# Optimization experiments

Measured on AMD Instinct MI355X. Metric: run time of the kernel, lower is better.

The kernel has to match this reference:

```python
import jax, jax.numpy as jnp
import numpy as np

# model constants (from source: PRE/COMM/OUT sizes; chosen: G, D, E, T, NF)
G, D, E, T = 128, 64, 8, 4096          # group feats, per-elevator feats, n elevators, timesteps
PRE, CI, CH, OUT, NF = 256, 128, 128, 128, 64
ROUNDS, DROPOFF = 3, 0.333
IN = G + D                              # elevator_input_size = 192
OIN = 2 * CH + IN                       # out-LSTM input = 448


def _cell(x, h, c, Wih, Whh, b):
    # torch nn.LSTM cell, gate order i,f,g,o; b = b_ih + b_hh
    g = x @ Wih.T + h @ Whh.T + b
    i, f, gg, o = jnp.split(g, 4, axis=-1)
    c2 = jax.nn.sigmoid(f) * c + jax.nn.sigmoid(i) * jnp.tanh(gg)
    h2 = jax.nn.sigmoid(o) * jnp.tanh(c2)
    return h2, c2


def _forward(features, pre_h0, pre_c0, out_h0, out_c0,
             Wih_p0, Whh_p0, b_p0, Wih_p1, Whh_p1, b_p1, Wfc, bfc,
             Wih_c0, Whh_c0, b_c0, Wih_c1, Whh_c1, b_c1,
             Wih_o, Whh_o, b_o, Wtar, btar, Wdir, bdir):
    def step(carry, feat):
        pre_h, pre_c, out_h, out_c = carry
        group = feat[:G]
        ele = feat[G:].reshape(E, D)
        x = jnp.concatenate([jnp.broadcast_to(group, (E, G)), ele], axis=-1)  # [E, IN]
        # preprocess: 2-layer LSTM single step, batched over elevators
        h0, c0 = _cell(x, pre_h[:, 0], pre_c[:, 0], Wih_p0, Whh_p0, b_p0)
        h1, c1 = _cell(h0, pre_h[:, 1], pre_c[:, 1], Wih_p1, Whh_p1, b_p1)
        pre_out = jax.nn.leaky_relu(h1 @ Wfc.T + bfc, 0.05)                   # [E, CI]
        new_pre_h = jnp.stack([h0, h1], axis=1)
        new_pre_c = jnp.stack([c0, c1], axis=1)
        # alpha-decayed communication rounds: sequential scan over elevators
        ch = jnp.zeros((2, CH), jnp.float32)
        cc = jnp.zeros((2, CH), jnp.float32)
        alpha = 1.0
        for _ in range(ROUNDS):
            def comm_step(cs, xin, alpha=alpha):
                ch_, cc_ = cs
                h0n, c0n = _cell(xin, ch_[0], cc_[0], Wih_c0, Whh_c0, b_c0)
                h0b = (1.0 - alpha) * ch_[0] + alpha * h0n
                c0b = (1.0 - alpha) * cc_[0] + alpha * c0n
                h1n, c1n = _cell(h0b, ch_[1], cc_[1], Wih_c1, Whh_c1, b_c1)
                h1b = (1.0 - alpha) * ch_[1] + alpha * h1n
                c1b = (1.0 - alpha) * cc_[1] + alpha * c1n
                return (jnp.stack([h0b, h1b]), jnp.stack([c0b, c1b])), None
            (ch, cc), _ = jax.lax.scan(comm_step, (ch, cc), pre_out)
            alpha *= DROPOFF
        group_dec = cc.reshape(-1)                                            # [2*CH] = comm_c.flatten()
        out_in = jnp.concatenate([jnp.broadcast_to(group_dec, (E, 2 * CH)), x], axis=-1)  # [E, OIN]
        oh, oc = _cell(out_in, out_h, out_c, Wih_o, Whh_o, b_o)
        tar = jax.nn.softmax(oh @ Wtar.T + btar, axis=-1)                     # [E, NF]
        dr = jax.nn.softmax(oh @ Wdir.T + bdir, axis=-1)                      # [E, 3]
        return (new_pre_h, new_pre_c, oh, oc), (tar, dr)

    _, (tar_seq, dir_seq) = jax.lax.scan(step, (pre_h0, pre_c0, out_h0, out_c0), features)
    return tar_seq, dir_seq


def setup_inputs() -> dict:
    key = jax.random.key(0)
    ks = iter(jax.random.split(key, 32))
    p = lambda *s: jax.random.normal(next(ks), s, jnp.float32) * 0.05
    return {
        "features": jax.random.normal(next(ks), (T, G + E * D), jnp.float32),
        "pre_h0": jnp.zeros((E, 2, PRE), jnp.float32),
        "pre_c0": jnp.zeros((E, 2, PRE), jnp.float32),
        "out_h0": jnp.zeros((E, OUT), jnp.float32),
        "out_c0": jnp.zeros((E, OUT), jnp.float32),
        "Wih_p0": p(4 * PRE, IN), "Whh_p0": p(4 * PRE, PRE), "b_p0": p(4 * PRE),
        "Wih_p1": p(4 * PRE, PRE), "Whh_p1": p(4 * PRE, PRE), "b_p1": p(4 * PRE),
        "Wfc": p(CI, PRE), "bfc": p(CI),
        "Wih_c0": p(4 * CH, CI), "Whh_c0": p(4 * CH, CH), "b_c0": p(4 * CH),
        "Wih_c1": p(4 * CH, CH), "Whh_c1": p(4 * CH, CH), "b_c1": p(4 * CH),
        "Wih_o": p(4 * OUT, OIN), "Whh_o": p(4 * OUT, OUT), "b_o": p(4 * OUT),
        "Wtar": p(NF, OUT), "btar": p(NF),
        "Wdir": p(3, OUT), "bdir": p(3),
    }


def reference(features, pre_h0, pre_c0, out_h0, out_c0,
              Wih_p0, Whh_p0, b_p0, Wih_p1, Whh_p1, b_p1, Wfc, bfc,
              Wih_c0, Whh_c0, b_c0, Wih_c1, Whh_c1, b_c1,
              Wih_o, Whh_o, b_o, Wtar, btar, Wdir, bdir):
    return _forward(features, pre_h0, pre_c0, out_h0, out_c0,
                    Wih_p0, Whh_p0, b_p0, Wih_p1, Whh_p1, b_p1, Wfc, bfc,
                    Wih_c0, Whh_c0, b_c0, Wih_c1, Whh_c1, b_c1,
                    Wih_o, Whh_o, b_o, Wtar, btar, Wdir, bdir)
```

## Files before the change

### kernel.cpp

```cpp
#include <hip/hip_runtime.h>
#include <hip/hip_bf16.h>

#define T_   4096
#define E_   8
#define NCON 56

typedef unsigned long long ull;

__device__ __forceinline__ float sigm(float x)  { return 1.0f / (1.0f + __expf(-x)); }
__device__ __forceinline__ float tanh_(float x) { return 1.0f - 2.0f / (__expf(2.0f * x) + 1.0f); }

__device__ __forceinline__ ull aload64(const ull* p) {
  return __hip_atomic_load(p, __ATOMIC_RELAXED, __HIP_MEMORY_SCOPE_AGENT);
}
__device__ __forceinline__ int aload32(const int* p) {
  return __hip_atomic_load(p, __ATOMIC_RELAXED, __HIP_MEMORY_SCOPE_AGENT);
}
__device__ __forceinline__ float aloadf(const float* p) {
  return __hip_atomic_load(p, __ATOMIC_RELAXED, __HIP_MEMORY_SCOPE_AGENT);
}
__device__ __forceinline__ float tagf(float h, unsigned g) {
  return __uint_as_float((__float_as_uint(h) & ~7u) | g);
}
__device__ __forceinline__ bool tagok4(const ull* v, unsigned g) {
  bool ok = true;
  #pragma unroll
  for (int i = 0; i < 4; ++i) {
    unsigned lo = (unsigned)v[i], hi = (unsigned)(v[i] >> 32);
    ok &= ((lo & 7u) == g) & ((hi & 7u) == g);
  }
  return ok;
}
__device__ __forceinline__ void lbar() {
  asm volatile("s_waitcnt lgkmcnt(0)\n\ts_barrier" ::: "memory");
}

#define FMA_8(ACC, W, VA, VB)                                   \
  ACC[0] = fmaf((W), (VA).x, ACC[0]); ACC[1] = fmaf((W), (VA).y, ACC[1]); \
  ACC[2] = fmaf((W), (VA).z, ACC[2]); ACC[3] = fmaf((W), (VA).w, ACC[3]); \
  ACC[4] = fmaf((W), (VB).x, ACC[4]); ACC[5] = fmaf((W), (VB).y, ACC[5]); \
  ACC[6] = fmaf((W), (VB).z, ACC[6]); ACC[7] = fmaf((W), (VB).w, ACC[7]);

__global__ void initK(const float* __restrict__ Wih_p0, const float* __restrict__ Whh_p0,
                      const float* __restrict__ Wih_p1, const float* __restrict__ Whh_p1,
                      const float* __restrict__ Wih_c0, const float* __restrict__ Whh_c0,
                      const float* __restrict__ Wih_c1, const float* __restrict__ Whh_c1,
                      const float* __restrict__ Wih_o,
                      float* wt_p0, float* wt_p1, float* wt_c0, float* wt_c1,
                      float* wt_o1, float* wt_o2, int* zbase) {
  const int NW = 458752 + 524288 + 131072 + 131072 + 131072 + 98304;
  const int NZ = 65536 + 16384 + 65536 + 16384;
  const int NTOT = NW + NZ;
  const int gsz = gridDim.x * blockDim.x;
  for (int i = blockIdx.x * blockDim.x + threadIdx.x; i < NTOT; i += gsz) {
    int idx = i;
    if (idx < 458752) { int k = idx >> 10, c = idx & 1023;
      int wg = c >> 5, r5 = c & 31, gate = r5 >> 3, jl = r5 & 7;
      int col = gate * 256 + wg * 8 + jl;
      wt_p0[idx] = (k < 192) ? Wih_p0[col * 192 + k] : Whh_p0[col * 256 + (k - 192)]; continue; }
    idx -= 458752;
    if (idx < 524288) { int k = idx >> 10, c = idx & 1023;
      int wg = c >> 5, r5 = c & 31, gate = r5 >> 3, jl = r5 & 7;
      int col = gate * 256 + wg * 8 + jl;
      wt_p1[idx] = (k < 256) ? Wih_p1[col * 256 + k] : Whh_p1[col * 256 + (k - 256)]; continue; }
    idx -= 524288;
    if (idx < 131072) { int k = idx >> 9, r = idx & 511;
      wt_c0[idx] = (k < 128) ? Wih_c0[r * 128 + k] : Whh_c0[r * 128 + (k - 128)]; continue; }
    idx -= 131072;
    if (idx < 131072) { int k = idx >> 9, r = idx & 511;
      wt_c1[idx] = (k < 128) ? Wih_c1[r * 128 + k] : Whh_c1[r * 128 + (k - 128)]; continue; }
    idx -= 131072;
    if (idx < 131072) { int k = idx >> 9, r = idx & 511;
      wt_o1[idx] = Wih_o[r * 448 + k]; continue; }
    idx -= 131072;
    if (idx < 98304) { int k = idx >> 9, r = idx & 511;
      wt_o2[idx] = Wih_o[r * 448 + 256 + k]; continue; }
    idx -= 98304;
    zbase[idx] = 0;
  }
}

__global__ void opre2K(const float* __restrict__ feat, const float* __restrict__ wt_o2,
                       __hip_bfloat16* __restrict__ opre2) {
  __shared__ float xb[192 * 8];
  const int t = blockIdx.x, tid = threadIdx.x;
  const float* ft = feat + (size_t)t * 640;
  for (int idx = tid; idx < 192 * 8; idx += 256) {
    int k = idx >> 3, e = idx & 7;
    xb[idx] = (k < 128) ? ft[k] : ft[128 + e * 64 + (k - 128)];
  }
  __syncthreads();
  const int r = tid;
  float A0[8] = {0,0,0,0,0,0,0,0};
  float A1[8] = {0,0,0,0,0,0,0,0};
  const float4* x4 = (const float4*)xb;
  #pragma unroll 2
  for (int k = 0; k < 192; ++k) {
    float w0 = wt_o2[k * 512 + r];
    float w1 = wt_o2[k * 512 + 256 + r];
    float4 a = x4[k * 2], b = x4[k * 2 + 1];
    FMA_8(A0, w0, a, b);
    FMA_8(A1, w1, a, b);
  }
  #pragma unroll
  for (int e = 0; e < 8; ++e) {
    opre2[((size_t)t * 8 + e) * 512 + r]       = __float2bfloat16(A0[e]);
    opre2[((size_t)t * 8 + e) * 512 + 256 + r] = __float2bfloat16(A1[e]);
  }
}

__device__ __forceinline__ void comm_cell(
    const float* __restrict__ wt, const float* __restrict__ bias,
    const float* xin, float* hL, float* cL, float* glb, float* hout,
    float alpha, int tid) {
  const int r = tid;
  float A0[8] = {0,0,0,0,0,0,0,0};
  float A1[8] = {0,0,0,0,0,0,0,0};
  const float4* x4 = (const float4*)xin;
  #pragma unroll 2
  for (int k = 0; k < 128; ++k) {
    float w0 = wt[k * 512 + r];
    float w1 = wt[k * 512 + 256 + r];
    float4 a = x4[k * 2], b = x4[k * 2 + 1];
    FMA_8(A0, w0, a, b);
    FMA_8(A1, w1, a, b);
  }
  const float4* h4 = (const float4*)hL;
  #pragma unroll 2
  for (int k = 0; k < 128; ++k) {
    float w0 = wt[(128 + k) * 512 + r];
    float w1 = wt[(128 + k) * 512 + 256 + r];
    float4 a = h4[k * 2], b = h4[k * 2 + 1];
    FMA_8(A0, w0, a, b);
    FMA_8(A1, w1, a, b);
  }
  {
    float4* g4 = (float4*)glb;
    g4[r * 2]             = make_float4(A0[0], A0[1], A0[2], A0[3]);
    g4[r * 2 + 1]         = make_float4(A0[4], A0[5], A0[6], A0[7]);
    g4[(256 + r) * 2]     = make_float4(A1[0], A1[1], A1[2], A1[3]);
    g4[(256 + r) * 2 + 1] = make_float4(A1[4], A1[5], A1[6], A1[7]);
  }
  __syncthreads();
  for (int idx = tid; idx < 1024; idx += 256) {
    int jj = idx >> 3, tt = idx & 7;
    float gi = glb[jj * 8 + tt]         + bias[jj];
    float gf = glb[(128 + jj) * 8 + tt] + bias[128 + jj];
    float gg = glb[(256 + jj) * 8 + tt] + bias[256 + jj];
    float go = glb[(384 + jj) * 8 + tt] + bias[384 + jj];
    float cold = cL[idx], hold = hL[idx];
    float c2 = sigm(gf) * cold + sigm(gi) * tanh_(gg);
    float h2 = sigm(go) * tanh_(c2);
    float hb = fmaf(alpha, h2 - hold, hold);
    float cb = fmaf(alpha, c2 - cold, cold);
    hL[idx] = hb; cL[idx] = cb;
    if (hout) hout[idx] = hb;
  }
  __syncthreads();
}

__launch_bounds__(256, 1)
__global__ void megaK(const float* __restrict__ feat,
                      const float* __restrict__ pre_h0, const float* __restrict__ pre_c0,
                      const float* __restrict__ wt_p0, const float* __restrict__ wt_p1,
                      const float* __restrict__ b_p0, const float* __restrict__ b_p1,
                      float* __restrict__ h0ring, float* __restrict__ h1ring,
                      float* __restrict__ h1all, int* __restrict__ flagsBC,
                      const float* __restrict__ Wfc, const float* __restrict__ bfc,
                      const float* __restrict__ wt_c0, const float* __restrict__ wt_c1,
                      const float* __restrict__ b_c0, const float* __restrict__ b_c1,
                      const float* __restrict__ wt_o1, const float* __restrict__ b_o,
                      float* __restrict__ opre1, int* __restrict__ flagC,
                      const __hip_bfloat16* __restrict__ opre2,
                      const float* __restrict__ Whh_o, const float* __restrict__ out_h0,
                      const float* __restrict__ out_c0, float* __restrict__ oh_g) {
  __shared__ float lds[38912];
  const int wg = blockIdx.x, tid = threadIdx.x;

  if (wg < 32) {
    float* wl  = lds;
    float* xb0 = lds + 14336;
    float* xb1 = lds + 15872;
    float* hsf = lds + 17408;
    float* gl  = lds + 19456;
    const int r5 = tid & 31, kq = tid >> 5;
    for (int idx = tid; idx < 14336; idx += 256)
      wl[idx] = wt_p0[(size_t)(idx >> 5) * 1024 + wg * 32 + (idx & 31)];
    float creg = 0.f, bi = 0.f, bff = 0.f, bg = 0.f, bo = 0.f;
    if (tid < 64) {
      const int jl = tid >> 3, e = tid & 7, j = wg * 8 + jl;
      creg = pre_c0[(e * 2 + 0) * 256 + j];
      bi = b_p0[j]; bff = b_p0[256 + j]; bg = b_p0[512 + j]; bo = b_p0[768 + j];
    }
    for (int idx = tid; idx < 2048; idx += 256) {
      int k = idx >> 3, e = idx & 7;
      hsf[idx] = pre_h0[(e * 2 + 0) * 256 + k];
    }
    for (int idx = tid; idx < 1536; idx += 256) {
      int k = idx >> 3, e = idx & 7;
      xb0[idx] = (k < 128) ? feat[k] : feat[128 + e * 64 + (k - 128)];
    }
    __syncthreads();
    const bool own = ((tid >> 3) == wg);
    float Ax[8] = {0,0,0,0,0,0,0,0};
    {
      const float4* x4 = (const float4*)xb0;
      #pragma unroll
      for (int k = kq * 24; k < kq * 24 + 24; ++k) {
        float w = wl[k * 32 + r5];
        float4 a = x4[k * 2], b = x4[k * 2 + 1];
        FMA_8(Ax, w, a, b);
      }
    }
    for (int t = 0; t < T_; ++t) {
      float px[6];
      if (t + 1 < T_) {
        const float* ft1 = feat + (size_t)(t + 1) * 640;
        #pragma unroll
        for (int i = 0; i < 6; ++i) {
          int idx = tid + i * 256; int k = idx >> 3, e = idx & 7;
          px[i] = (k < 128) ? ft1[k] : ft1[128 + e * 64 + (k - 128)];
        }
      }
      float A[8];
      #pragma unroll
      for (int i = 0; i < 8; ++i) A[i] = Ax[i];
      {
        const float4* h4 = (const float4*)hsf;
        #pragma unroll
        for (int k2 = 0; k2 < 32; ++k2) {
          const int k = kq * 32 + k2;
          float w = wl[(192 + k) * 32 + r5];
          float4 a = h4[k * 2], b = h4[k * 2 + 1];
          FMA_8(A, w, a, b);
        }
      }
      {
        float4* g4 = (float4*)gl;
        g4[(kq * 32 + r5) * 2]     = make_float4(A[0], A[1], A[2], A[3]);
        g4[(kq * 32 + r5) * 2 + 1] = make_float4(A[4], A[5], A[6], A[7]);
      }
      if (t + 1 < T_) {
        float* xbN = ((t + 1) & 1) ? xb1 : xb0;
        #pragma unroll
        for (int i = 0; i < 6; ++i) xbN[tid + i * 256] = px[i];
      }
      if (t >= 24 && tid >= 224) {
        const int t2 = (t - 24) | 7;
        const int* fp = flagsBC + ((size_t)(t2 & 63) * 32 + (tid - 224)) * 32;
        while (aload32(fp) < t2 + 1) __builtin_amdgcn_s_sleep(16);
      }
      lbar();
      const unsigned g = ((unsigned)(t >> 5) % 7u) + 1u;
      float* ringS = h0ring + (size_t)(t & 31) * 2048;
      if (tid < 64) {
        float s0 = 0.f, s1 = 0.f, s2 = 0.f, s3 = 0.f;
        #pragma unroll
        for (int q = 0; q < 8; ++q) {
          s0 += gl[q * 256 + tid];       s1 += gl[q * 256 + 64 + tid];
          s2 += gl[q * 256 + 128 + tid]; s3 += gl[q * 256 + 192 + tid];
        }
        float c2 = sigm(s1 + bff) * creg + sigm(s0 + bi) * tanh_(s2 + bg);
        float h2 = sigm(s3 + bo) * tanh_(c2);
        creg = c2;
        __hip_atomic_store(&ringS[wg * 64 + tid], tagf(h2, g),
                           __ATOMIC_RELAXED, __HIP_MEMORY_SCOPE_AGENT);
        hsf[wg * 64 + tid] = h2;
      }
      if (t + 1 >= T_) break;
      ull v[4];
      const ull* rp = (const ull*)ringS + tid * 4;
      if (!own) {
        #pragma unroll
        for (int i = 0; i < 4; ++i) v[i] = aload64(rp + i);
      }
      #pragma unroll
      for (int i = 0; i < 8; ++i) Ax[i] = 0.f;
      {
        const float4* x4 = (const float4*)(((t + 1) & 1) ? xb1 : xb0);
        #pragma unroll
        for (int k = kq * 24; k < kq * 24 + 24; ++k) {
          float w = wl[k * 32 + r5];
          float4 a = x4[k * 2], b = x4[k * 2 + 1];
          FMA_8(Ax, w, a, b);
        }
      }
      if (!own) {
        while (!tagok4(v, g)) {
          __builtin_amdgcn_s_sleep(1);
          #pragma unroll
          for (int i = 0; i < 4; ++i) v[i] = aload64(rp + i);
        }
        ull* d8 = (ull*)hsf;
        #pragma unroll
        for (int i = 0; i < 4; ++i) d8[tid * 4 + i] = v[i];
      }
      lbar();
    }
  } else if (wg < 64) {
    const int wgl = wg - 32;
    float* wl  = lds;
    float* xh0 = lds + 16384;
    float* hsf = lds + 18432;
    float* gl  = lds + 20480;
    const int r5 = tid & 31, kq = tid >> 5;
    for (int idx = tid; idx < 16384; idx += 256)
      wl[idx] = wt_p1[(size_t)(idx >> 5) * 1024 + wgl * 32 + (idx & 31)];
    float creg = 0.f, bi = 0.f, bff = 0.f, bg = 0.f, bo = 0.f;
    if (tid < 64) {
      const int jl = tid >> 3, e = tid & 7, j = wgl * 8 + jl;
      creg = pre_c0[(e * 2 + 1) * 256 + j];
      bi = b_p1[j]; bff = b_p1[256 + j]; bg = b_p1[512 + j]; bo = b_p1[768 + j];
    }
    for (int idx = tid; idx < 2048; idx += 256) {
      int k = idx >> 3, e = idx & 7;
      hsf[idx] = pre_h0[(e * 2 + 1) * 256 + k];
    }
    __syncthreads();
    const bool own = ((tid >> 3) == wgl);
    ull pv[4];
    {
      ull v[4];
      const ull* rp = (const ull*)h0ring + tid * 4;
      #pragma unroll
      for (int i = 0; i < 4; ++i) v[i] = aload64(rp + i);
      while (!tagok4(v, 1u)) {
        __builtin_amdgcn_s_sleep(1);
        #pragma unroll
        for (int i = 0; i < 4; ++i) v[i] = aload64(rp + i);
      }
      ull* d8 = (ull*)xh0;
      #pragma unroll
      for (int i = 0; i < 4; ++i) d8[tid * 4 + i] = v[i];
    }
    lbar();
    float Ax[8] = {0,0,0,0,0,0,0,0};
    {
      const float4* x4 = (const float4*)xh0;
      #pragma unroll
      for (int k = kq * 32; k < kq * 32 + 32; ++k) {
        float w = wl[k * 32 + r5];
        float4 a = x4[k * 2], b = x4[k * 2 + 1];
        FMA_8(Ax, w, a, b);
      }
    }
    {
      const ull* rp = (const ull*)(h0ring + 2048) + tid * 4;
      #pragma unroll
      for (int i = 0; i < 4; ++i) pv[i] = aload64(rp + i);
      while (!tagok4(pv, 1u)) {
        __builtin_amdgcn_s_sleep(1);
        #pragma unroll
        for (int i = 0; i < 4; ++i) pv[i] = aload64(rp + i);
      }
    }
    lbar();
    for (int t = 0; t < T_; ++t) {
      float A[8];
      #pragma unroll
      for (int i = 0; i < 8; ++i) A[i] = Ax[i];
      {
        const float4* h4 = (const float4*)hsf;
        #pragma unroll
        for (int k2 = 0; k2 < 32; ++k2) {
          const int k = kq * 32 + k2;
          float w = wl[(256 + k) * 32 + r5];
          float4 a = h4[k * 2], b = h4[k * 2 + 1];
          FMA_8(A, w, a, b);
        }
      }
      {
        float4* g4 = (float4*)gl;
        g4[(kq * 32 + r5) * 2]     = make_float4(A[0], A[1], A[2], A[3]);
        g4[(kq * 32 + r5) * 2 + 1] = make_float4(A[4], A[5], A[6], A[7]);
      }
      if (t + 1 < T_) {
        ull* d8 = (ull*)xh0;
        #pragma unroll
        for (int i = 0; i < 4; ++i) d8[tid * 4 + i] = pv[i];
      }
      lbar();
      const unsigned g1 = ((unsigned)(t >> 3) % 7u) + 1u;
      float* ringS = h1ring + (size_t)(t & 7) * 2048;
      if (tid < 64) {
        float s0 = 0.f, s1 = 0.f, s2 = 0.f, s3 = 0.f;
        #pragma unroll
        for (int q = 0; q < 8; ++q) {
          s0 += gl[q * 256 + tid];       s1 += gl[q * 256 + 64 + tid];
          s2 += gl[q * 256 + 128 + tid]; s3 += gl[q * 256 + 192 + tid];
        }
        float c2 = sigm(s1 + bff) * creg + sigm(s0 + bi) * tanh_(s2 + bg);
        float h2 = sigm(s3 + bo) * tanh_(c2);
        creg = c2;
        __hip_atomic_store(&ringS[wgl * 64 + tid], tagf(h2, g1),
                           __ATOMIC_RELAXED, __HIP_MEMORY_SCOPE_AGENT);
        hsf[wgl * 64 + tid] = h2;
        __hip_atomic_store(&h1all[(size_t)t * 2048 + wgl * 64 + tid], h2,
                           __ATOMIC_RELAXED, __HIP_MEMORY_SCOPE_AGENT);
        if ((t & 7) == 7) {
          asm volatile("s_waitcnt vmcnt(0)" ::: "memory");
          if (tid == 0)
            __hip_atomic_store(&flagsBC[((size_t)(t & 63) * 32 + wgl) * 32], t + 1,
                               __ATOMIC_RELAXED, __HIP_MEMORY_SCOPE_AGENT);
        }
      }
      if (t + 1 >= T_) break;
      ull w1[4];
      const ull* rp1 = (const ull*)ringS + tid * 4;
      if (!own) {
        #pragma unroll
        for (int i = 0; i < 4; ++i) w1[i] = aload64(rp1 + i);
      }
      #pragma unroll
      for (int i = 0; i < 8; ++i) Ax[i] = 0.f;
      {
        const float4* x4 = (const float4*)xh0;
        #pragma unroll
        for (int k = kq * 32; k < kq * 32 + 32; ++k) {
          float w = wl[k * 32 + r5];
          float4 a = x4[k * 2], b = x4[k * 2 + 1];
          FMA_8(Ax, w, a, b);
        }
      }
      if (!own) {
        while (!tagok4(w1, g1)) {
          __builtin_amdgcn_s_sleep(1);
          #pragma unroll
          for (int i = 0; i < 4; ++i) w1[i] = aload64(rp1 + i);
        }
        ull* d8 = (ull*)hsf;
        #pragma unroll
        for (int i = 0; i < 4; ++i) d8[tid * 4 + i] = w1[i];
      }
      if (t + 2 < T_) {
        const unsigned g0 = ((unsigned)((t + 2) >> 5) % 7u) + 1u;
        const ull* rp0 = (const ull*)(h0ring + (size_t)((t + 2) & 31) * 2048) + tid * 4;
        #pragma unroll
        for (int i = 0; i < 4; ++i) pv[i] = aload64(rp0 + i);
        while (!tagok4(pv, g0)) {
          __builtin_amdgcn_s_sleep(1);
          #pragma unroll
          for (int i = 0; i < 4; ++i) pv[i] = aload64(rp0 + i);
        }
      }
      lbar();
    }
  } else if (wg < 72) {
    const int e = wg - 64;
    float* wlds = lds;
    float* ohl  = lds + 32768;
    float* gl   = lds + 32896;
    for (int idx = tid; idx < 32768; idx += 256) {
      int k = idx >> 8, rr = idx & 255;
      wlds[idx] = Whh_o[(256 + rr) * 128 + k];
    }
    float w[128];
    #pragma unroll
    for (int k = 0; k < 128; ++k) w[k] = Whh_o[tid * 128 + k];
    if (tid < 128) ohl[tid] = out_h0[e * 128 + tid];
    float creg = (tid < 128) ? out_c0[e * 128 + tid] : 0.f;
    __syncthreads();
    if (tid == 0) { while (aload32(&flagC[0]) == 0) __builtin_amdgcn_s_sleep(4); }
    __syncthreads();
    const int r0 = tid, r1 = tid + 256;
    float pa = aloadf(&opre1[r0]), pb = aloadf(&opre1[r1]);
    float qa = __bfloat162float(opre2[(size_t)e * 512 + r0]);
    float qb = __bfloat162float(opre2[(size_t)e * 512 + r1]);
    float na = aloadf(&opre1[512 + r0]), nb = aloadf(&opre1[512 + r1]);
    float ma = __bfloat162float(opre2[(size_t)(8 + e) * 512 + r0]);
    float mb = __bfloat162float(opre2[(size_t)(8 + e) * 512 + r1]);
    for (int t = 0; t < T_; ++t) {
      float a0 = pa + qa, a1 = pb + qb;
      pa = na; pb = nb; qa = ma; qb = mb;
      if ((t & 7) == 6 && t + 2 < T_) {
        if (tid == 0) { while (aload32(&flagC[((t + 2) >> 3) * 32]) == 0) __builtin_amdgcn_s_sleep(4); }
        __syncthreads();
      }
      if (t + 2 < T_) {
        na = aloadf(&opre1[(size_t)(t + 2) * 512 + r0]);
        nb = aloadf(&opre1[(size_t)(t + 2) * 512 + r1]);
        ma = __bfloat162float(opre2[((size_t)(t + 2) * 8 + e) * 512 + r0]);
        mb = __bfloat162float(opre2[((size_t)(t + 2) * 8 + e) * 512 + r1]);
      }
      const float4* o4 = (const float4*)ohl;
      #pragma unroll
      for (int kk = 0; kk < 32; ++kk) {
        float4 x = o4[kk];
        a0 = fmaf(w[kk * 4 + 0], x.x, a0); a0 = fmaf(w[kk * 4 + 1], x.y, a0);
        a0 = fmaf(w[kk * 4 + 2], x.z, a0); a0 = fmaf(w[kk * 4 + 3], x.w, a0);
        a1 = fmaf(wlds[(kk * 4 + 0) * 256 + tid], x.x, a1);
        a1 = fmaf(wlds[(kk * 4 + 1) * 256 + tid], x.y, a1);
        a1 = fmaf(wlds[(kk * 4 + 2) * 256 + tid], x.z, a1);
        a1 = fmaf(wlds[(kk * 4 + 3) * 256 + tid], x.w, a1);
      }
      gl[r0] = a0; gl[r1] = a1;
      __syncthreads();
      if (tid < 128) {
        float gi = gl[tid], gf = gl[128 + tid], gg = gl[256 + tid], go = gl[384 + tid];
        float c2 = sigm(gf) * creg + sigm(gi) * tanh_(gg);
        float h2 = sigm(go) * tanh_(c2);
        creg = c2;
        ohl[tid] = h2;
        oh_g[(size_t)t * 1024 + e * 128 + tid] = h2;
      }
      __syncthreads();
    }
  } else {
    const int cb = wg - 72;
    float* h1c    = lds;
    float* polAll = lds + 16384;
    float* ch0 = lds + 24576; float* cc0 = lds + 25600;
    float* ch1 = lds + 26624; float* cc1 = lds + 27648;
    float* h0b = lds + 28672;
    float* glb = lds + 29696;
    for (int chunk = cb; chunk < 512; chunk += NCON) {
      const int t0 = chunk * 8;
      if (tid < 32) {
        const int* fp = flagsBC + ((size_t)((t0 + 7) & 63) * 32 + tid) * 32;
        while (aload32(fp) < t0 + 8) __builtin_amdgcn_s_sleep(64);
      }
      __syncthreads();
      {
        const ull* src = (const ull*)(h1all + (size_t)t0 * 2048);
        ull* dst = (ull*)h1c;
        for (int i = tid; i < 8192; i += 256) dst[i] = aload64(src + i);
      }
      __syncthreads();
      {
        const int c = tid >> 1, half = tid & 1;
        const float bv = bfc[c];
        const float* wrow = Wfc + c * 256;
        for (int tt = 0; tt < 8; ++tt) {
          float a0 = bv, a1 = bv, a2 = bv, a3 = bv;
          const float4* h4 = (const float4*)(h1c + tt * 2048);
          #pragma unroll 4
          for (int k = 0; k < 256; ++k) {
            float wv = wrow[k];
            float4 x = h4[k * 2 + half];
            a0 = fmaf(wv, x.x, a0); a1 = fmaf(wv, x.y, a1);
            a2 = fmaf(wv, x.z, a2); a3 = fmaf(wv, x.w, a3);
          }
          float vv[4] = {a0, a1, a2, a3};
          #pragma unroll
          for (int i = 0; i < 4; ++i) {
            float v = vv[i];
            v = (v > 0.f) ? v : 0.05f * v;
            polAll[(half * 4 + i) * 1024 + c * 8 + tt] = v;
          }
        }
      }
      for (int idx = tid; idx < 1024; idx += 256) { ch0[idx]=0.f; cc0[idx]=0.f; ch1[idx]=0.f; cc1[idx]=0.f; }
      __syncthreads();
      float alpha = 1.0f;
      for (int rd = 0; rd < 3; ++rd) {
        for (int e = 0; e < E_; ++e) {
          comm_cell(wt_c0, b_c0, polAll + e * 1024, ch0, cc0, glb, h0b, alpha, tid);
          comm_cell(wt_c1, b_c1, h0b, ch1, cc1, glb, nullptr, alpha, tid);
        }
        alpha *= 0.333f;
      }
      {
        const int r = tid;
        float A0[8], A1[8];
        #pragma unroll
        for (int tt = 0; tt < 8; ++tt) { A0[tt] = b_o[r]; A1[tt] = b_o[256 + r]; }
        const float4* c04 = (const float4*)cc0;
        const float4* c14 = (const float4*)cc1;
        #pragma unroll 2
        for (int k = 0; k < 128; ++k) {
          float w0 = wt_o1[k * 512 + r], w1 = wt_o1[k * 512 + 256 + r];
          float4 a = c04[k * 2], b = c04[k * 2 + 1];
          FMA_8(A0, w0, a, b);
          FMA_8(A1, w1, a, b);
        }
        #pragma unroll 2
        for (int k = 0; k < 128; ++k) {
          float w0 = wt_o1[(128 + k) * 512 + r], w1 = wt_o1[(128 + k) * 512 + 256 + r];
          float4 a = c14[k * 2], b = c14[k * 2 + 1];
          FMA_8(A0, w0, a, b);
          FMA_8(A1, w1, a, b);
        }
        #pragma unroll
        for (int tt = 0; tt < 8; ++tt) {
          __hip_atomic_store(&opre1[((size_t)(t0 + tt)) * 512 + r], A0[tt],
                             __ATOMIC_RELAXED, __HIP_MEMORY_SCOPE_AGENT);
          __hip_atomic_store(&opre1[((size_t)(t0 + tt)) * 512 + 256 + r], A1[tt],
                             __ATOMIC_RELAXED, __HIP_MEMORY_SCOPE_AGENT);
        }
      }
      __syncthreads();
      if (tid == 0)
        __hip_atomic_store(&flagC[chunk * 32], 1, __ATOMIC_RELAXED, __HIP_MEMORY_SCOPE_AGENT);
      __syncthreads();
    }
  }
}

__global__ void phaseD(const float* __restrict__ oh_g,
                       const float* __restrict__ Wtar, const float* __restrict__ btar,
                       const float* __restrict__ Wdir, const float* __restrict__ bdir,
                       float* __restrict__ outp) {
  __shared__ float ohl[1024];
  const int t = blockIdx.x, tid = threadIdx.x;
  for (int idx = tid; idx < 1024; idx += 64) ohl[idx] = oh_g[(size_t)t * 1024 + idx];
  __syncthreads();
  const int f = tid;
  for (int e = 0; e < E_; ++e) {
    float acc = btar[f];
    const float* wr = Wtar + f * 128;
    #pragma unroll 4
    for (int k = 0; k < 128; ++k) acc = fmaf(wr[k], ohl[e * 128 + k], acc);
    float m = acc;
    #pragma unroll
    for (int off = 32; off; off >>= 1) m = fmaxf(m, __shfl_xor(m, off, 64));
    float ex = __expf(acc - m);
    float s = ex;
    #pragma unroll
    for (int off = 32; off; off >>= 1) s += __shfl_xor(s, off, 64);
    outp[((size_t)t * 8 + e) * 64 + f] = ex / s;
  }
  if (tid < 8) {
    int e = tid;
    float d0 = bdir[0], d1 = bdir[1], d2 = bdir[2];
    #pragma unroll 4
    for (int k = 0; k < 128; ++k) {
      float x = ohl[e * 128 + k];
      d0 = fmaf(Wdir[k], x, d0);
      d1 = fmaf(Wdir[128 + k], x, d1);
      d2 = fmaf(Wdir[256 + k], x, d2);
    }
    float m = fmaxf(d0, fmaxf(d1, d2));
    float x0 = __expf(d0 - m), x1 = __expf(d1 - m), x2 = __expf(d2 - m);
    float s = x0 + x1 + x2;
    float* dp = outp + (size_t)T_ * 8 * 64 + ((size_t)t * 8 + e) * 3;
    dp[0] = x0 / s; dp[1] = x1 / s; dp[2] = x2 / s;
  }
}

extern "C" void kernel_launch(void* const* d_in, const int* in_sizes, int n_in,
                              void* d_out, int out_size, void* d_ws, size_t ws_size,
                              hipStream_t stream) {
  (void)in_sizes; (void)n_in; (void)out_size; (void)ws_size;
  const float* feat   = (const float*)d_in[0];
  const float* pre_h0 = (const float*)d_in[1];
  const float* pre_c0 = (const float*)d_in[2];
  const float* out_h0 = (const float*)d_in[3];
  const float* out_c0 = (const float*)d_in[4];
  const float* Wih_p0 = (const float*)d_in[5];
  const float* Whh_p0 = (const float*)d_in[6];
  const float* b_p0   = (const float*)d_in[7];
  const float* Wih_p1 = (const float*)d_in[8];
  const float* Whh_p1 = (const float*)d_in[9];
  const float* b_p1   = (const float*)d_in[10];
  const float* Wfc    = (const float*)d_in[11];
  const float* bfc    = (const float*)d_in[12];
  const float* Wih_c0 = (const float*)d_in[13];
  const float* Whh_c0 = (const float*)d_in[14];
  const float* b_c0   = (const float*)d_in[15];
  const float* Wih_c1 = (const float*)d_in[16];
  const float* Whh_c1 = (const float*)d_in[17];
  const float* b_c1   = (const float*)d_in[18];
  const float* Wih_o  = (const float*)d_in[19];
  const float* Whh_o  = (const float*)d_in[20];
  const float* b_o    = (const float*)d_in[21];
  const float* Wtar   = (const float*)d_in[22];
  const float* btar   = (const float*)d_in[23];
  const float* Wdir   = (const float*)d_in[24];
  const float* bdir   = (const float*)d_in[25];
  float* outp = (float*)d_out;

  float* ws = (float*)d_ws;
  size_t off = 0;
  float* opre1    = ws + off; off += (size_t)T_ * 512;
  float* oh_g     = ws + off; off += (size_t)T_ * E_ * 128;
  float* wt_p0    = ws + off; off += (size_t)448 * 1024;
  float* wt_p1    = ws + off; off += (size_t)512 * 1024;
  float* wt_c0    = ws + off; off += (size_t)256 * 512;
  float* wt_c1    = ws + off; off += (size_t)256 * 512;
  float* wt_o1    = ws + off; off += (size_t)256 * 512;
  float* wt_o2    = ws + off; off += (size_t)192 * 512;
  __hip_bfloat16* opre2 = (__hip_bfloat16*)(ws + off);
  off += (size_t)T_ * E_ * 512 / 2;
  float* h1all  = ws + off; off += (size_t)T_ * 2048;
  float* h0ring = ws + off; off += (size_t)32 * 2048;
  float* h1ring = ws + off; off += (size_t)8 * 2048;
  int* flags    = (int*)(ws + off);
  int* flagsBC  = flags;
  int* flagC    = flags + (size_t)64 * 32 * 32;
  int* zbase    = (int*)h0ring;

  initK<<<dim3(1024), dim3(256), 0, stream>>>(
      Wih_p0, Whh_p0, Wih_p1, Whh_p1, Wih_c0, Whh_c0, Wih_c1, Whh_c1, Wih_o,
      wt_p0, wt_p1, wt_c0, wt_c1, wt_o1, wt_o2, zbase);
  opre2K<<<dim3(T_), dim3(256), 0, stream>>>(feat, wt_o2, opre2);
  megaK<<<dim3(32 + 32 + 8 + NCON), dim3(256), 0, stream>>>(
      feat, pre_h0, pre_c0, wt_p0, wt_p1, b_p0, b_p1,
      h0ring, h1ring, h1all, flagsBC,
      Wfc, bfc, wt_c0, wt_c1, b_c0, b_c1, wt_o1, b_o, opre1, flagC,
      opre2, Whh_o, out_h0, out_c0, oh_g);
  phaseD<<<dim3(T_), dim3(64), 0, stream>>>(oh_g, Wtar, btar, Wdir, bdir, outp);
}
```

Before: 15.78 ms.

## Interleave megakernel roles across XCDs and duplicate h0 ring for cross-role reads

```diff
diff --git a/kernel.cpp b/kernel.cpp
--- a/kernel.cpp
+++ b/kernel.cpp
@@ -49,7 +49,7 @@
                       float* wt_p0, float* wt_p1, float* wt_c0, float* wt_c1,
                       float* wt_o1, float* wt_o2, int* zbase) {
   const int NW = 458752 + 524288 + 131072 + 131072 + 131072 + 98304;
-  const int NZ = 65536 + 16384 + 65536 + 16384;
+  const int NZ = 65536 + 65536 + 16384 + 65536 + 16384;
   const int NTOT = NW + NZ;
   const int gsz = gridDim.x * blockDim.x;
   for (int i = blockIdx.x * blockDim.x + threadIdx.x; i < NTOT; i += gsz) {
@@ -164,7 +164,8 @@
                       const float* __restrict__ pre_h0, const float* __restrict__ pre_c0,
                       const float* __restrict__ wt_p0, const float* __restrict__ wt_p1,
                       const float* __restrict__ b_p0, const float* __restrict__ b_p1,
-                      float* __restrict__ h0ring, float* __restrict__ h1ring,
+                      float* __restrict__ h0ringL, float* __restrict__ h0ringG,
+                      float* __restrict__ h1ringL,
                       float* __restrict__ h1all, int* __restrict__ flagsBC,
                       const float* __restrict__ Wfc, const float* __restrict__ bfc,
                       const float* __restrict__ wt_c0, const float* __restrict__ wt_c1,
@@ -175,30 +176,32 @@
                       const float* __restrict__ Whh_o, const float* __restrict__ out_h0,
                       const float* __restrict__ out_c0, float* __restrict__ oh_g) {
   __shared__ float lds[38912];
-  const int wg = blockIdx.x, tid = threadIdx.x;
-
-  if (wg < 32) {
+  const int role = blockIdx.x & 7, idx = blockIdx.x >> 3;
+  const int tid = threadIdx.x;
+
+  if (role == 0) {
+    const int wg = idx;
     float* wl  = lds;
     float* xb0 = lds + 14336;
     float* xb1 = lds + 15872;
     float* hsf = lds + 17408;
     float* gl  = lds + 19456;
     const int r5 = tid & 31, kq = tid >> 5;
-    for (int idx = tid; idx < 14336; idx += 256)
-      wl[idx] = wt_p0[(size_t)(idx >> 5) * 1024 + wg * 32 + (idx & 31)];
+    for (int i2 = tid; i2 < 14336; i2 += 256)
+      wl[i2] = wt_p0[(size_t)(i2 >> 5) * 1024 + wg * 32 + (i2 & 31)];
     float creg = 0.f, bi = 0.f, bff = 0.f, bg = 0.f, bo = 0.f;
     if (tid < 64) {
       const int jl = tid >> 3, e = tid & 7, j = wg * 8 + jl;
       creg = pre_c0[(e * 2 + 0) * 256 + j];
       bi = b_p0[j]; bff = b_p0[256 + j]; bg = b_p0[512 + j]; bo = b_p0[768 + j];
     }
-    for (int idx = tid; idx < 2048; idx += 256) {
-      int k = idx >> 3, e = idx & 7;
-      hsf[idx] = pre_h0[(e * 2 + 0) * 256 + k];
-    }
-    for (int idx = tid; idx < 1536; idx += 256) {
-      int k = idx >> 3, e = idx & 7;
-      xb0[idx] = (k < 128) ? feat[k] : feat[128 + e * 64 + (k - 128)];
+    for (int i2 = tid; i2 < 2048; i2 += 256) {
+      int k = i2 >> 3, e = i2 & 7;
+      hsf[i2] = pre_h0[(e * 2 + 0) * 256 + k];
+    }
+    for (int i2 = tid; i2 < 1536; i2 += 256) {
+      int k = i2 >> 3, e = i2 & 7;
+      xb0[i2] = (k < 128) ? feat[k] : feat[128 + e * 64 + (k - 128)];
     }
     __syncthreads();
     const bool own = ((tid >> 3) == wg);
@@ -218,7 +221,7 @@
         const float* ft1 = feat + (size_t)(t + 1) * 640;
         #pragma unroll
         for (int i = 0; i < 6; ++i) {
-          int idx = tid + i * 256; int k = idx >> 3, e = idx & 7;
+          int i2 = tid + i * 256; int k = i2 >> 3, e = i2 & 7;
           px[i] = (k < 128) ? ft1[k] : ft1[128 + e * 64 + (k - 128)];
         }
       }
@@ -252,7 +255,7 @@
       }
       lbar();
       const unsigned g = ((unsigned)(t >> 5) % 7u) + 1u;
-      float* ringS = h0ring + (size_t)(t & 31) * 2048;
+      float* ringS = h0ringL + (size_t)(t & 31) * 2048;
       if (tid < 64) {
         float s0 = 0.f, s1 = 0.f, s2 = 0.f, s3 = 0.f;
         #pragma unroll
@@ -263,7 +266,10 @@
         float c2 = sigm(s1 + bff) * creg + sigm(s0 + bi) * tanh_(s2 + bg);
         float h2 = sigm(s3 + bo) * tanh_(c2);
         creg = c2;
-        __hip_atomic_store(&ringS[wg * 64 + tid], tagf(h2, g),
+        float tv = tagf(h2, g);
+        __hip_atomic_store(&ringS[wg * 64 + tid], tv,
+                           __ATOMIC_RELAXED, __HIP_MEMORY_SCOPE_AGENT);
+        __hip_atomic_store(&h0ringG[(size_t)(t & 31) * 2048 + wg * 64 + tid], tv,
                            __ATOMIC_RELAXED, __HIP_MEMORY_SCOPE_AGENT);
         hsf[wg * 64 + tid] = h2;
       }
@@ -297,31 +303,31 @@
       }
       lbar();
     }
-  } else if (wg < 64) {
-    const int wgl = wg - 32;
+  } else if (role == 1) {
+    const int wgl = idx;
     float* wl  = lds;
     float* xh0 = lds + 16384;
     float* hsf = lds + 18432;
     float* gl  = lds + 20480;
     const int r5 = tid & 31, kq = tid >> 5;
-    for (int idx = tid; idx < 16384; idx += 256)
-      wl[idx] = wt_p1[(size_t)(idx >> 5) * 1024 + wgl * 32 + (idx & 31)];
+    for (int i2 = tid; i2 < 16384; i2 += 256)
+      wl[i2] = wt_p1[(size_t)(i2 >> 5) * 1024 + wgl * 32 + (i2 & 31)];
     float creg = 0.f, bi = 0.f, bff = 0.f, bg = 0.f, bo = 0.f;
     if (tid < 64) {
       const int jl = tid >> 3, e = tid & 7, j = wgl * 8 + jl;
       creg = pre_c0[(e * 2 + 1) * 256 + j];
       bi = b_p1[j]; bff = b_p1[256 + j]; bg = b_p1[512 + j]; bo = b_p1[768 + j];
     }
-    for (int idx = tid; idx < 2048; idx += 256) {
-      int k = idx >> 3, e = idx & 7;
-      hsf[idx] = pre_h0[(e * 2 + 1) * 256 + k];
+    for (int i2 = tid; i2 < 2048; i2 += 256) {
+      int k = i2 >> 3, e = i2 & 7;
+      hsf[i2] = pre_h0[(e * 2 + 1) * 256 + k];
     }
     __syncthreads();
     const bool own = ((tid >> 3) == wgl);
     ull pv[4];
     {
       ull v[4];
-      const ull* rp = (const ull*)h0ring + tid * 4;
+      const ull* rp = (const ull*)h0ringG + tid * 4;
       #pragma unroll
       for (int i = 0; i < 4; ++i) v[i] = aload64(rp + i);
       while (!tagok4(v, 1u)) {
@@ -345,7 +351,7 @@
       }
     }
     {
-      const ull* rp = (const ull*)(h0ring + 2048) + tid * 4;
+      const ull* rp = (const ull*)(h0ringG + 2048) + tid * 4;
       #pragma unroll
       for (int i = 0; i < 4; ++i) pv[i] = aload64(rp + i);
       while (!tagok4(pv, 1u)) {
@@ -381,7 +387,7 @@
       }
       lbar();
       const unsigned g1 = ((unsigned)(t >> 3) % 7u) + 1u;
-      float* ringS = h1ring + (size_t)(t & 7) * 2048;
+      float* ringS = h1ringL + (size_t)(t & 7) * 2048;
       if (tid < 64) {
         float s0 = 0.f, s1 = 0.f, s2 = 0.f, s3 = 0.f;
         #pragma unroll
@@ -434,7 +440,7 @@
       }
       if (t + 2 < T_) {
         const unsigned g0 = ((unsigned)((t + 2) >> 5) % 7u) + 1u;
-        const ull* rp0 = (const ull*)(h0ring + (size_t)((t + 2) & 31) * 2048) + tid * 4;
+        const ull* rp0 = (const ull*)(h0ringG + (size_t)((t + 2) & 31) * 2048) + tid * 4;
         #pragma unroll
         for (int i = 0; i < 4; ++i) pv[i] = aload64(rp0 + i);
         while (!tagok4(pv, g0)) {
@@ -445,14 +451,14 @@
       }
       lbar();
     }
-  } else if (wg < 72) {
-    const int e = wg - 64;
+  } else if (role == 2 && idx < 8) {
+    const int e = idx;
     float* wlds = lds;
     float* ohl  = lds + 32768;
     float* gl   = lds + 32896;
-    for (int idx = tid; idx < 32768; idx += 256) {
-      int k = idx >> 8, rr = idx & 255;
-      wlds[idx] = Whh_o[(256 + rr) * 128 + k];
+    for (int i2 = tid; i2 < 32768; i2 += 256) {
+      int k = i2 >> 8, rr = i2 & 255;
+      wlds[i2] = Whh_o[(256 + rr) * 128 + k];
     }
     float w[128];
     #pragma unroll
@@ -505,8 +511,9 @@
       }
       __syncthreads();
     }
-  } else {
-    const int cb = wg - 72;
+  } else if (role >= 3) {
+    const int cb = (role - 3) * 32 + idx;
+    if (cb >= NCON) return;
     float* h1c    = lds;
     float* polAll = lds + 16384;
     float* ch0 = lds + 24576; float* cc0 = lds + 25600;
@@ -549,7 +556,7 @@
           }
         }
       }
-      for (int idx = tid; idx < 1024; idx += 256) { ch0[idx]=0.f; cc0[idx]=0.f; ch1[idx]=0.f; cc1[idx]=0.f; }
+      for (int i2 = tid; i2 < 1024; i2 += 256) { ch0[i2]=0.f; cc0[i2]=0.f; ch1[i2]=0.f; cc1[i2]=0.f; }
       __syncthreads();
       float alpha = 1.0f;
       for (int rd = 0; rd < 3; ++rd) {
@@ -681,21 +688,22 @@
   float* wt_o2    = ws + off; off += (size_t)192 * 512;
   __hip_bfloat16* opre2 = (__hip_bfloat16*)(ws + off);
   off += (size_t)T_ * E_ * 512 / 2;
-  float* h1all  = ws + off; off += (size_t)T_ * 2048;
-  float* h0ring = ws + off; off += (size_t)32 * 2048;
-  float* h1ring = ws + off; off += (size_t)8 * 2048;
+  float* h1all   = ws + off; off += (size_t)T_ * 2048;
+  float* h0ringL = ws + off; off += (size_t)32 * 2048;
+  float* h0ringG = ws + off; off += (size_t)32 * 2048;
+  float* h1ringL = ws + off; off += (size_t)8 * 2048;
   int* flags    = (int*)(ws + off);
   int* flagsBC  = flags;
   int* flagC    = flags + (size_t)64 * 32 * 32;
-  int* zbase    = (int*)h0ring;
+  int* zbase    = (int*)h0ringL;
 
   initK<<<dim3(1024), dim3(256), 0, stream>>>(
       Wih_p0, Whh_p0, Wih_p1, Whh_p1, Wih_c0, Whh_c0, Wih_c1, Whh_c1, Wih_o,
       wt_p0, wt_p1, wt_c0, wt_c1, wt_o1, wt_o2, zbase);
   opre2K<<<dim3(T_), dim3(256), 0, stream>>>(feat, wt_o2, opre2);
-  megaK<<<dim3(32 + 32 + 8 + NCON), dim3(256), 0, stream>>>(
+  megaK<<<dim3(256), dim3(256), 0, stream>>>(
       feat, pre_h0, pre_c0, wt_p0, wt_p1, b_p0, b_p1,
-      h0ring, h1ring, h1all, flagsBC,
+      h0ringL, h0ringG, h1ringL, h1all, flagsBC,
       Wfc, bfc, wt_c0, wt_c1, b_c0, b_c1, wt_o1, b_o, opre1, flagC,
       opre2, Whh_o, out_h0, out_c0, oh_g);
   phaseD<<<dim3(T_), dim3(64), 0, stream>>>(oh_g, Wtar, btar, Wdir, bdir, outp);
```

New measurement: 15.56 ms. Within noise of the previous version (-1.4%).
